# Performance work log

Hardware: AMD Instinct MI355X
Metric: run time of the kernel (lower is better)

The kernel has to match this reference:

```python
import jax, jax.numpy as jnp
import numpy as np

NUM_UNITS = 64
NUM_HEADS = 12
MODEL_UNITS = NUM_UNITS * NUM_HEADS  # 768, must equal input feature dim for residual
EPS = 1e-7  # K.epsilon()


def setup_inputs() -> dict:
    key = jax.random.key(0)
    ks = jax.random.split(key, 7)
    B, T, D = 8, 1024, MODEL_UNITS
    x = jax.random.normal(ks[0], (B, T, D), dtype=jnp.float32)
    mask = jnp.ones((B, T), dtype=bool)
    w_q = jax.random.normal(ks[1], (D, MODEL_UNITS), dtype=jnp.float32) * (D ** -0.5)
    w_k = jax.random.normal(ks[2], (D, MODEL_UNITS), dtype=jnp.float32) * (D ** -0.5)
    w_v = jax.random.normal(ks[3], (D, MODEL_UNITS), dtype=jnp.float32) * (D ** -0.5)
    w_final = jax.random.normal(ks[4], (MODEL_UNITS, MODEL_UNITS), dtype=jnp.float32) * (MODEL_UNITS ** -0.5)
    gamma = jnp.ones((MODEL_UNITS,), dtype=jnp.float32)
    beta = jnp.zeros((MODEL_UNITS,), dtype=jnp.float32)
    return {"x": x, "mask": mask, "w_q": w_q, "w_k": w_k, "w_v": w_v,
            "w_final": w_final, "gamma": gamma, "beta": beta}


def reference(x, mask, w_q, w_k, w_v, w_final, gamma, beta):
    B, T, D = x.shape
    H, U = NUM_HEADS, NUM_UNITS
    # Project and split into heads. Keras split(axis=2) -> head h takes cols h*U:(h+1)*U,
    # which is exactly a reshape [B,T,H,U].
    q = (x @ w_q).reshape(B, T, H, U)
    k = (x @ w_k).reshape(B, T, H, U)
    v = (x @ w_v).reshape(B, T, H, U)
    scale = D ** (-0.5)
    # scores: [B,H,T,T]
    scores = jnp.einsum('bthu,bshu->bhts', q, k) * scale
    m = mask.astype(x.dtype)  # [B,T]
    scores = scores * m[:, None, None, :]  # mask keys
    scores = scores * m[:, None, :, None]  # mask queries
    # sum-normalization (NOT softmax), per source
    scores = scores / (jnp.sum(scores, axis=-1, keepdims=True) + EPS)
    out = jnp.einsum('bhts,bshu->bthu', scores, v).reshape(B, T, H * U)
    out = out @ w_final
    out = out + x  # residual
    # faithful reproduction of source 'normalization' (std is assigned mean — source bug)
    mean = jnp.mean(out, axis=-1, keepdims=True)
    std = mean
    out = gamma * (out - mean) / (std + EPS) + beta
    return out
```

## Files before the change

### kernel.cpp

```cpp
#include <hip/hip_runtime.h>

#define NB 8
#define NT 1024
#define ND 768
#define NH 12
#define NU 64
#define BT (NB*NT)
#define SCALE32 ((float)0.03608439182435161)
#define EPS32 1e-7f

__device__ __forceinline__ float dot64_np(const float* a, const float* b)
{
    float r[4];
#pragma unroll
    for (int j = 0; j < 4; j++) r[j] = __fmul_rn(a[j], b[j]);
#pragma unroll
    for (int i = 1; i < 16; i++)
#pragma unroll
        for (int j = 0; j < 4; j++)
            r[j] = __fadd_rn(r[j], __fmul_rn(a[i * 4 + j], b[i * 4 + j]));
    return __fadd_rn(__fadd_rn(r[0], r[2]), __fadd_rn(r[1], r[3]));
}

__global__ __launch_bounds__(256) void mask_k(
    const unsigned char* __restrict__ mb, float* __restrict__ mf)
{
    __shared__ int cntOff, cntAll;
    if (threadIdx.x == 0) { cntOff = 0; cntAll = 0; }
    __syncthreads();
    int lo = 0, la = 0;
    for (int i = threadIdx.x; i < BT; i += 256)
        if (mb[i] != 0) { la++; if ((i & 3) != 0) lo++; }
    atomicAdd(&cntOff, lo);
    atomicAdd(&cntAll, la);
    __syncthreads();
    const bool int32mode = (cntOff == 0) && (cntAll != 0);
    if (int32mode) {
        const int* mi = (const int*)mb;
        for (int i = threadIdx.x; i < BT; i += 256)
            mf[i] = (mi[i] != 0) ? 1.f : 0.f;
    } else {
        for (int i = threadIdx.x; i < BT; i += 256)
            mf[i] = (mb[i] != 0) ? 1.f : 0.f;
    }
}

__global__ __launch_bounds__(256) void gemmseq(
    const float* __restrict__ A, const float* __restrict__ W,
    const float* __restrict__ R, float* __restrict__ C)
{
    __shared__ float sA[64][132];
    __shared__ float sB[64][68];

    const int t = threadIdx.x;
    const int mbase = blockIdx.x * 128;
    const int nbase = blockIdx.y * 64;
    const int m0 = (t >> 4) * 8;
    const int n0 = (t & 15) * 4;

    float acc[8][4], accA[8][4];
#pragma unroll
    for (int i = 0; i < 8; i++)
#pragma unroll
        for (int j = 0; j < 4; j++) { acc[i][j] = 0.f; accA[i][j] = 0.f; }

    for (int k0 = 0; k0 < 768; k0 += 64) {
        __syncthreads();
#pragma unroll
        for (int i = 0; i < 8; i++) {
            const int idx = t + i * 256;
            const int ar = idx >> 4;
            const int ak4 = (idx & 15) * 4;
            const float4 a4 = *(const float4*)&A[(size_t)(mbase + ar) * 768 + k0 + ak4];
            sA[ak4 + 0][ar] = a4.x;
            sA[ak4 + 1][ar] = a4.y;
            sA[ak4 + 2][ar] = a4.z;
            sA[ak4 + 3][ar] = a4.w;
        }
#pragma unroll
        for (int i = 0; i < 4; i++) {
            const int idx = t + i * 256;
            const int br = idx >> 4;
            const int bk4 = (idx & 15) * 4;
            *(float4*)&sB[br][bk4] =
                *(const float4*)&W[(size_t)(k0 + br) * 768 + nbase + bk4];
        }
        __syncthreads();

        for (int kk = 0; kk < 64; kk++) {
            float av[8], bv[4];
            *(float4*)&av[0] = *(const float4*)&sA[kk][m0];
            *(float4*)&av[4] = *(const float4*)&sA[kk][m0 + 4];
            *(float4*)&bv[0] = *(const float4*)&sB[kk][n0];
#pragma unroll
            for (int i = 0; i < 8; i++)
#pragma unroll
                for (int j = 0; j < 4; j++)
                    acc[i][j] = fmaf(av[i], bv[j], acc[i][j]);
        }

        if (k0 + 64 == 384) {
#pragma unroll
            for (int i = 0; i < 8; i++)
#pragma unroll
                for (int j = 0; j < 4; j++) {
                    accA[i][j] = acc[i][j];
                    acc[i][j] = 0.f;
                }
        }
    }

#pragma unroll
    for (int i = 0; i < 8; i++)
#pragma unroll
        for (int j = 0; j < 4; j++) {
            const size_t idx = (size_t)(mbase + m0 + i) * 768 + nbase + n0 + j;
            float o = __fadd_rn(accA[i][j], acc[i][j]);
            if (R) o = __fadd_rn(o, R[idx]);
            C[idx] = o;
        }
}

__global__ __launch_bounds__(128) void denom_np(
    const float* __restrict__ Q, const float* __restrict__ K,
    const float* __restrict__ MF, float* __restrict__ D)
{
    const int bid = blockIdx.x;
    const int lb  = (bid & 7) * 96 + (bid >> 3);
    const int gid = lb * 128 + threadIdx.x;
    const int bh = gid >> 10;
    const int row = gid & 1023;
    const int b = bh / NH, h = bh % NH;
    const int bh_u = __builtin_amdgcn_readfirstlane(bh);
    const int b_u = bh_u / NH, h_u = bh_u % NH;

    const float mq = MF[b * NT + row];

    float qr[64];
    const float4* qp = (const float4*)&Q[((size_t)(b * NT + row)) * ND + h * 64];
#pragma unroll
    for (int i = 0; i < 16; i++) *(float4*)&qr[i * 4] = qp[i];

    const float* Kb = &K[((size_t)(b_u * NT)) * ND + h_u * 64];
    const float* MFb = &MF[b_u * NT];

    float Bi[8];
    for (int c = 0; c < 8; c++) {
        float b8[8];
        for (int s = 0; s < 128; s++) {
            const int sg = c * 128 + s;
            const float dt = dot64_np(qr, Kb + (size_t)sg * ND);
            float sc = __fmul_rn(dt, SCALE32);
            sc = __fmul_rn(sc, MFb[sg]);
            sc = __fmul_rn(sc, mq);
            const int j = s & 7;
            if (s < 8) b8[j] = sc;
            else       b8[j] = __fadd_rn(b8[j], sc);
        }
        Bi[c] = __fadd_rn(__fadd_rn(__fadd_rn(b8[0], b8[1]), __fadd_rn(b8[2], b8[3])),
                          __fadd_rn(__fadd_rn(b8[4], b8[5]), __fadd_rn(b8[6], b8[7])));
    }

    D[(size_t)bh * NT + row] = __fadd_rn(
        __fadd_rn(__fadd_rn(Bi[0], Bi[1]), __fadd_rn(Bi[2], Bi[3])),
        __fadd_rn(__fadd_rn(Bi[4], Bi[5]), __fadd_rn(Bi[6], Bi[7])));
}

__global__ __launch_bounds__(128) void attn_np(
    const float* __restrict__ K, const float* __restrict__ V,
    const float* __restrict__ D, const float* __restrict__ MF,
    float* __restrict__ QA)
{
    const int bid = blockIdx.x;
    const int lb  = (bid & 7) * 96 + (bid >> 3);
    const int gid = lb * 128 + threadIdx.x;
    const int bh = gid >> 10;
    const int row = gid & 1023;
    const int b = bh / NH, h = bh % NH;
    const int bh_u = __builtin_amdgcn_readfirstlane(bh);
    const int b_u = bh_u / NH, h_u = bh_u % NH;

    const float mq = MF[b * NT + row];
    const float De = __fadd_rn(D[(size_t)bh * NT + row], EPS32);

    float qr[64];
    const float4* qp = (const float4*)&QA[((size_t)(b * NT + row)) * ND + h * 64];
#pragma unroll
    for (int i = 0; i < 16; i++) *(float4*)&qr[i * 4] = qp[i];

    float o[64];
#pragma unroll
    for (int j = 0; j < 64; j++) o[j] = 0.f;

    const float* Kb = &K[((size_t)(b_u * NT)) * ND + h_u * 64];
    const float* Vb = &V[((size_t)(b_u * NT)) * ND + h_u * 64];
    const float* MFb = &MF[b_u * NT];

    for (int s = 0; s < NT; s++) {
        const float dt = dot64_np(qr, Kb + (size_t)s * ND);
        float sc = __fmul_rn(dt, SCALE32);
        sc = __fmul_rn(sc, MFb[s]);
        sc = __fmul_rn(sc, mq);
        const float p = __fdiv_rn(sc, De);
        const float* vp = Vb + (size_t)s * ND;
#pragma unroll
        for (int j = 0; j < 64; j++)
            o[j] = __fadd_rn(o[j], __fmul_rn(p, vp[j]));
    }

    float4* op = (float4*)&QA[((size_t)(b * NT + row)) * ND + h * 64];
#pragma unroll
    for (int i = 0; i < 16; i++) op[i] = *(float4*)&o[i * 4];
}

__global__ __launch_bounds__(256) void rownorm_np(
    float* __restrict__ Y, const float* __restrict__ gamma,
    const float* __restrict__ beta)
{
    const int wave = threadIdx.x >> 6, lane = threadIdx.x & 63;
    const int row = blockIdx.x * 4 + wave;
    float* yr = Y + (size_t)row * ND;
    const int c = lane >> 3, j = lane & 7;

    const float* a = yr + c * 96;
    float r = a[j];
#pragma unroll
    for (int i = 1; i < 12; i++) r = __fadd_rn(r, a[i * 8 + j]);

    r = __fadd_rn(r, __shfl_xor(r, 1, 64));
    r = __fadd_rn(r, __shfl_xor(r, 2, 64));
    r = __fadd_rn(r, __shfl_xor(r, 4, 64));
    r = __fadd_rn(r, __shfl_xor(r, 8, 64));
    r = __fadd_rn(r, __shfl_xor(r, 16, 64));
    r = __fadd_rn(r, __shfl_xor(r, 32, 64));

    const float m = __fdiv_rn(r, 768.0f);
    const float mpe = __fadd_rn(m, EPS32);

#pragma unroll
    for (int i = 0; i < 12; i++) {
        const int idx = i * 64 + lane;
        const float v = yr[idx];
        float o = __fsub_rn(v, m);
        o = __fmul_rn(gamma[idx], o);
        o = __fdiv_rn(o, mpe);
        o = __fadd_rn(o, beta[idx]);
        yr[idx] = o;
    }
}

extern "C" void kernel_launch(void* const* d_in, const int* in_sizes, int n_in,
                              void* d_out, int out_size, void* d_ws, size_t ws_size,
                              hipStream_t stream)
{
    (void)in_sizes; (void)n_in; (void)out_size; (void)ws_size;
    const float* x     = (const float*)d_in[0];
    const unsigned char* maskb = (const unsigned char*)d_in[1];
    const float* wq    = (const float*)d_in[2];
    const float* wk    = (const float*)d_in[3];
    const float* wv    = (const float*)d_in[4];
    const float* wf    = (const float*)d_in[5];
    const float* gamma = (const float*)d_in[6];
    const float* beta  = (const float*)d_in[7];

    float* ws = (float*)d_ws;
    float* MF = ws;
    float* D  = MF + BT;
    float* Q  = D + (size_t)96 * NT;
    float* K  = Q + (size_t)BT * ND;
    float* V  = K + (size_t)BT * ND;
    float* Y  = (float*)d_out;

    mask_k<<<1, 256, 0, stream>>>(maskb, MF);
    gemmseq<<<dim3(64, 12), 256, 0, stream>>>(x, wq, nullptr, Q);
    gemmseq<<<dim3(64, 12), 256, 0, stream>>>(x, wk, nullptr, K);
    gemmseq<<<dim3(64, 12), 256, 0, stream>>>(x, wv, nullptr, V);
    denom_np<<<768, 128, 0, stream>>>(Q, K, MF, D);
    attn_np<<<768, 128, 0, stream>>>(K, V, D, MF, Q);
    gemmseq<<<dim3(64, 12), 256, 0, stream>>>(Q, wf, x, Y);
    rownorm_np<<<2048, 256, 0, stream>>>(Y, gamma, beta);
}
```

Measured before the change: 1.725 ms.

## Double-buffer shared-memory tiles in projection GEMM with register prefetch

The GEMM now splits K into 32-wide tiles held in two shared-memory buffers. The next tile's global loads are issued into registers before the current tile is computed, then written to the other buffer. This aims to hide global load latency behind FMA work and drop one barrier per iteration. It costs extra registers for the prefetch buffers and runs more, shorter K iterations.

```diff
diff --git a/kernel.cpp b/kernel.cpp
--- a/kernel.cpp
+++ b/kernel.cpp
@@ -49,8 +49,8 @@
     const float* __restrict__ A, const float* __restrict__ W,
     const float* __restrict__ R, float* __restrict__ C)
 {
-    __shared__ float sA[64][132];
-    __shared__ float sB[64][68];
+    __shared__ float sA[2][32][132];
+    __shared__ float sB[2][32][68];
 
     const int t = threadIdx.x;
     const int mbase = blockIdx.x * 128;
@@ -58,40 +58,61 @@
     const int m0 = (t >> 4) * 8;
     const int n0 = (t & 15) * 4;
 
+
     float acc[8][4], accA[8][4];
 #pragma unroll
     for (int i = 0; i < 8; i++)
 #pragma unroll
         for (int j = 0; j < 4; j++) { acc[i][j] = 0.f; accA[i][j] = 0.f; }
 
-    for (int k0 = 0; k0 < 768; k0 += 64) {
-        __syncthreads();
-#pragma unroll
-        for (int i = 0; i < 8; i++) {
-            const int idx = t + i * 256;
-            const int ar = idx >> 4;
-            const int ak4 = (idx & 15) * 4;
-            const float4 a4 = *(const float4*)&A[(size_t)(mbase + ar) * 768 + k0 + ak4];
-            sA[ak4 + 0][ar] = a4.x;
-            sA[ak4 + 1][ar] = a4.y;
-            sA[ak4 + 2][ar] = a4.z;
-            sA[ak4 + 3][ar] = a4.w;
-        }
-#pragma unroll
-        for (int i = 0; i < 4; i++) {
-            const int idx = t + i * 256;
-            const int br = idx >> 4;
-            const int bk4 = (idx & 15) * 4;
-            *(float4*)&sB[br][bk4] =
-                *(const float4*)&W[(size_t)(k0 + br) * 768 + nbase + bk4];
-        }
-        __syncthreads();
-
-        for (int kk = 0; kk < 64; kk++) {
+#pragma unroll
+    for (int i = 0; i < 4; i++) {
+        const int idx = t + i * 256;
+        const int mr = idx >> 3;
+        const int k4 = (idx & 7) * 4;
+        const float4 a4 = *(const float4*)&A[(size_t)(mbase + mr) * 768 + k4];
+        sA[0][k4 + 0][mr] = a4.x;
+        sA[0][k4 + 1][mr] = a4.y;
+        sA[0][k4 + 2][mr] = a4.z;
+        sA[0][k4 + 3][mr] = a4.w;
+    }
+#pragma unroll
+    for (int i = 0; i < 2; i++) {
+        const int idx = t + i * 256;
+        const int br = idx >> 4;
+        const int bn4 = (idx & 15) * 4;
+        *(float4*)&sB[0][br][bn4] =
+            *(const float4*)&W[(size_t)br * 768 + nbase + bn4];
+    }
+    __syncthreads();
+
+    for (int kt = 0; kt < 24; kt++) {
+        const int cur = kt & 1;
+
+        float4 ra[4], rb[2];
+        if (kt + 1 < 24) {
+            const int k0n = (kt + 1) * 32;
+#pragma unroll
+            for (int i = 0; i < 4; i++) {
+                const int idx = t + i * 256;
+                const int mr = idx >> 3;
+                const int k4 = (idx & 7) * 4;
+                ra[i] = *(const float4*)&A[(size_t)(mbase + mr) * 768 + k0n + k4];
+            }
+#pragma unroll
+            for (int i = 0; i < 2; i++) {
+                const int idx = t + i * 256;
+                const int br = idx >> 4;
+                const int bn4 = (idx & 15) * 4;
+                rb[i] = *(const float4*)&W[(size_t)(k0n + br) * 768 + nbase + bn4];
+            }
+        }
+
+        for (int kk = 0; kk < 32; kk++) {
             float av[8], bv[4];
-            *(float4*)&av[0] = *(const float4*)&sA[kk][m0];
-            *(float4*)&av[4] = *(const float4*)&sA[kk][m0 + 4];
-            *(float4*)&bv[0] = *(const float4*)&sB[kk][n0];
+            *(float4*)&av[0] = *(const float4*)&sA[cur][kk][m0];
+            *(float4*)&av[4] = *(const float4*)&sA[cur][kk][m0 + 4];
+            *(float4*)&bv[0] = *(const float4*)&sB[cur][kk][n0];
 #pragma unroll
             for (int i = 0; i < 8; i++)
 #pragma unroll
@@ -99,7 +120,7 @@
                     acc[i][j] = fmaf(av[i], bv[j], acc[i][j]);
         }
 
-        if (k0 + 64 == 384) {
+        if (kt == 11) {
 #pragma unroll
             for (int i = 0; i < 8; i++)
 #pragma unroll
@@ -107,6 +128,27 @@
                     accA[i][j] = acc[i][j];
                     acc[i][j] = 0.f;
                 }
+        }
+
+        if (kt + 1 < 24) {
+#pragma unroll
+            for (int i = 0; i < 4; i++) {
+                const int idx = t + i * 256;
+                const int mr = idx >> 3;
+                const int k4 = (idx & 7) * 4;
+                sA[cur ^ 1][k4 + 0][mr] = ra[i].x;
+                sA[cur ^ 1][k4 + 1][mr] = ra[i].y;
+                sA[cur ^ 1][k4 + 2][mr] = ra[i].z;
+                sA[cur ^ 1][k4 + 3][mr] = ra[i].w;
+            }
+#pragma unroll
+            for (int i = 0; i < 2; i++) {
+                const int idx = t + i * 256;
+                const int br = idx >> 4;
+                const int bn4 = (idx & 15) * 4;
+                *(float4*)&sB[cur ^ 1][br][bn4] = rb[i];
+            }
+            __syncthreads();
         }
     }
 
```

Result: no change. 1.707 ms (-1.0%).
